# Performance work log

Measured on AMD Instinct MI355X. Metric: run time of the kernel, lower is better.

Reference implementation:

```python
import jax, jax.numpy as jnp
import numpy as np

B, T, V, E, H, NC = 256, 512, 128, 128, 256, 10000


def setup_inputs() -> dict:
    key = jax.random.key(0)
    ks = jax.random.split(key, 10)
    return {
        "dec_input_batch": jax.random.randint(ks[0], (B, T), 0, V),
        "dec_input_lengths": jax.random.randint(ks[1], (B,), 1, T + 1),
        "max_prob_clusters": jax.random.randint(ks[2], (B,), 0, NC),
        "char_embeddings": jax.random.normal(ks[3], (V, E), dtype=jnp.float32) * 0.1,
        "cluster_embeddings": jax.random.normal(ks[4], (NC, H), dtype=jnp.float32) * 0.1,
        "W0": jax.random.normal(ks[5], (E + H + H, 4 * H), dtype=jnp.float32) * 0.05,
        "b0": jnp.zeros((4 * H,), jnp.float32),
        "W1": jax.random.normal(ks[6], (H + H, 4 * H), dtype=jnp.float32) * 0.05,
        "b1": jnp.zeros((4 * H,), jnp.float32),
        "decoderW": jax.random.normal(ks[7], (H, V), dtype=jnp.float32) * (1.0 / (H + V)),
        "decoderB": jnp.zeros((V,), jnp.float32),
    }


def _lstm_step(c, h, x, W, b):
    # TF BasicLSTMCell: gates order i, j, f, o; forget_bias = 1.0
    z = jnp.concatenate([x, h], axis=-1) @ W + b
    i, j, f, o = jnp.split(z, 4, axis=-1)
    c2 = c * jax.nn.sigmoid(f + 1.0) + jax.nn.sigmoid(i) * jnp.tanh(j)
    h2 = jnp.tanh(c2) * jax.nn.sigmoid(o)
    return c2, h2


def reference(dec_input_batch, dec_input_lengths, max_prob_clusters,
              char_embeddings, cluster_embeddings, W0, b0, W1, b1,
              decoderW, decoderB):
    Bb, Tt = dec_input_batch.shape
    Hh = decoderW.shape[0]
    x = char_embeddings[dec_input_batch]                       # [B,T,E]
    clus = cluster_embeddings[max_prob_clusters]               # [B,H]
    clus_bt = jnp.broadcast_to(clus[:, None, :], (Bb, Tt, clus.shape[-1]))
    x = jnp.concatenate([x, clus_bt], axis=-1)                 # [B,T,E+H]
    xs = jnp.transpose(x, (1, 0, 2))                           # [T,B,E+H]
    # dynamic_rnn sequence_length semantics: past length -> zero output, state copied through
    mask = (jnp.arange(Tt)[:, None] < dec_input_lengths[None, :])[..., None]  # [T,B,1]
    zeros = jnp.zeros((Bb, Hh), x.dtype)

    def step(carry, inp):
        c0, h0, c1, h1 = carry
        xt, m = inp
        c0n, h0n = _lstm_step(c0, h0, xt, W0, b0)
        c1n, h1n = _lstm_step(c1, h1, h0n, W1, b1)
        c0 = jnp.where(m, c0n, c0); h0 = jnp.where(m, h0n, h0)
        c1 = jnp.where(m, c1n, c1); h1 = jnp.where(m, h1n, h1)
        out = jnp.where(m, h1n, jnp.zeros_like(h1n))
        return (c0, h0, c1, h1), out

    _, outs = jax.lax.scan(step, (zeros, zeros, zeros, zeros), (xs, mask))
    outs = jnp.transpose(outs, (1, 0, 2))                      # [B,T,H]
    raw_scores = outs @ decoderW + decoderB                    # [B,T,V]
    return raw_scores
```

## Files before the change

### kernel.cpp

```cpp
#include <hip/hip_runtime.h>

#define B_ 256
#define T_ 512
#define V_ 128
#define E_ 128
#define H_ 256
#define FH 1024

#define GROUPS 32
#define RPG 8
#define CWG 16
#define NWG (GROUPS*CWG)

#define HTG 2048
#define GST (GROUPS*HTG)

typedef float f4 __attribute__((ext_vector_type(4)));

#define OFF_HT0  0
#define OFF_HT1  (OFF_HT0 + 2*GST)
#define OFF_BAR  (OFF_HT1 + 2*GST)
#define BARSZ    (GROUPS*1024)
#define OFF_TP   (OFF_BAR + BARSZ)
#define OFF_CP   (OFF_TP + V_*FH)
#define OFF_WP0  (OFF_CP + B_*FH)
#define OFF_WP1  (OFF_WP0 + CWG*64*64*4)
#define OFF_DWT  (OFF_WP1 + CWG*128*64*4)
#define OFF_B1   (OFF_DWT + V_*H_)
#define OFF_PERM (OFF_B1 + FH)

__device__ __forceinline__ int gcol(int c, int col) {
  int u = col >> 2, g = col & 3;
  return g*256 + c*16 + u;
}

__device__ __forceinline__ float sigm(float x){ return 1.f/(1.f+__expf(-x)); }
__device__ __forceinline__ float tanh_(float x){ return 1.f - 2.f/(1.f+__expf(2.f*x)); }


__global__ void prep_pack(const float* __restrict__ W0, const float* __restrict__ W1,
                          const float* __restrict__ dW, const float* __restrict__ b1,
                          float* __restrict__ ws) {
  float* wp0 = ws + OFF_WP0; float* wp1 = ws + OFF_WP1;
  float* dwT = ws + OFF_DWT; float* b1p = ws + OFF_B1;
  const int N0 = CWG*64*64*4;
  const int N1 = CWG*128*64*4;
  const int N2 = V_*H_;
  const int N3 = FH;
  const int total = N0+N1+N2+N3;
  for (int i = blockIdx.x*blockDim.x + threadIdx.x; i < total; i += gridDim.x*blockDim.x) {
    if (i < N0) {
      int cc = i >> 14; int rem = i & 16383;
      int kb = rem >> 8; int ln = (rem >> 2) & 63; int j = i & 3;
      int k = kb*4 + j;
      wp0[i] = W0[(E_+H_+k)*FH + gcol(cc, ln)];
    } else if (i < N0+N1) {
      int idx = i - N0;
      int cc = idx >> 15; int rem = idx & 32767;
      int kb = rem >> 8; int ln = (rem >> 2) & 63; int j = idx & 3;
      int k2 = kb*4 + j;
      wp1[idx] = W1[k2*FH + gcol(cc, ln)];
    } else if (i < N0+N1+N2) {
      int l = i - N0 - N1;
      int v = l >> 8, k = l & 255;
      dwT[l] = dW[k*V_ + v];
    } else {
      int cc2 = i - N0 - N1 - N2;
      b1p[cc2] = b1[gcol(cc2>>6, cc2&63)];
    }
  }
}

__global__ void prep_tok(const float* __restrict__ cemb, const float* __restrict__ W0,
                         float* __restrict__ ws) {
  __shared__ float ce[E_];
  float* TP = ws + OFF_TP;
  int v = blockIdx.x >> 2, q = blockIdx.x & 3;
  int tid = threadIdx.x;
  if (tid < E_) ce[tid] = cemb[v*E_ + tid];
  __syncthreads();
  int ccol = q*256 + tid;
  int G = gcol(ccol>>6, ccol&63);
  float acc = 0.f;
  for (int e = 0; e < E_; ++e) acc = fmaf(ce[e], W0[e*FH + G], acc);
  TP[v*FH + ccol] = acc;
}

__global__ void prep_clus(const int* __restrict__ clus, const float* __restrict__ clemb,
                          const float* __restrict__ W0, const float* __restrict__ b0,
                          float* __restrict__ ws) {
  __shared__ float ce[H_];
  float* CP = ws + OFF_CP;
  int b = blockIdx.x >> 2, q = blockIdx.x & 3;
  int tid = threadIdx.x;
  int cl = clus[b];
  ce[tid] = clemb[(long long)cl*H_ + tid];
  __syncthreads();
  int ccol = q*256 + tid;
  int G = gcol(ccol>>6, ccol&63);
  float acc = b0[G];
  for (int e = 0; e < H_; ++e) acc = fmaf(ce[e], W0[(E_+e)*FH + G], acc);
  CP[b*FH + ccol] = acc;
}

__global__ void prep_sort(const int* __restrict__ lens, float* __restrict__ ws) {
  __shared__ int sl[B_];
  int* perm = (int*)(ws + OFF_PERM);
  const int i = threadIdx.x;
  sl[i] = lens[i];
  __syncthreads();
  const int li = sl[i];
  int rank = 0;
  for (int j = 0; j < B_; ++j) {
    const int lj = sl[j];
    rank += (lj > li) || (lj == li && j < i);
  }
  perm[rank] = i;
}


__device__ __forceinline__ void st64(float* p, float a, float b) {
  float2 t; t.x = a; t.y = b;
  __hip_atomic_store((unsigned long long*)p, __builtin_bit_cast(unsigned long long, t),
                     __ATOMIC_RELAXED, __HIP_MEMORY_SCOPE_AGENT);
}

__device__ __forceinline__ unsigned long long ld64(const void* p) {
  return __hip_atomic_load((const unsigned long long*)p, __ATOMIC_RELAXED,
                           __HIP_MEMORY_SCOPE_AGENT);
}

__device__ __forceinline__ void flag_set(unsigned* p, unsigned v) {
  asm volatile("s_waitcnt vmcnt(0)" ::: "memory");
  __hip_atomic_store(p, v, __ATOMIC_RELAXED, __HIP_MEMORY_SCOPE_AGENT);
}

__device__ __forceinline__ void spinAB(const unsigned* fgrp, int lane, unsigned tgt) {
  const unsigned* p = fgrp + (lane & 15)*32 + ((lane >> 5) << 4);
  unsigned v = __hip_atomic_load(p, __ATOMIC_RELAXED, __HIP_MEMORY_SCOPE_AGENT);
  while (!__all((int)(v >= tgt))) {
    __builtin_amdgcn_s_sleep(4);
    v = __hip_atomic_load(p, __ATOMIC_RELAXED, __HIP_MEMORY_SCOPE_AGENT);
  }
}

__device__ __forceinline__ void spinB(const unsigned* fgrp, int lane, unsigned tgt) {
  const unsigned* p = fgrp + (lane & 15)*32 + 16;
  unsigned v = __hip_atomic_load(p, __ATOMIC_RELAXED, __HIP_MEMORY_SCOPE_AGENT);
  while (!__all((int)(v >= tgt))) {
    __builtin_amdgcn_s_sleep(4);
    v = __hip_atomic_load(p, __ATOMIC_RELAXED, __HIP_MEMORY_SCOPE_AGENT);
  }
}

__device__ __forceinline__ void lstm_gate(const f4 z, float& cc, float& hh, const bool upd) {
  float ci = sigm(z.x);
  float cj = tanh_(z.y);
  float cf = sigm(z.z + 1.f);
  float co = sigm(z.w);
  float cn = fmaf(cc, cf, ci*cj);
  float hn = tanh_(cn)*co;
  if (upd) { cc = cn; hh = hn; }
}


__global__ __launch_bounds__(256, 2) void lstm_persist(
    const int* __restrict__ toks, const int* __restrict__ lens,
    const float* __restrict__ decB, float* __restrict__ ws, float* __restrict__ out)
{
  const int blk  = blockIdx.x;
  const int xcd  = blk & 7;
  const int j    = blk >> 3;
  const int grp  = (xcd << 2) | ((j & 1) << 1) | (j >> 5);
  const int c    = (j >> 1) & 15;
  const int tid  = threadIdx.x;
  const int lane = tid & 63;
  const int wv   = tid >> 6;
  const int cof  = c*64;

  const int sgrp  = ((grp & 3) << 3) | (grp >> 2);
  const int rbase = sgrp*RPG;
  const int* perm = (const int*)(ws + OFF_PERM);

  float* ht0 = ws + OFF_HT0;
  float* ht1 = ws + OFF_HT1;
  unsigned* fgrp = (unsigned*)(ws + OFF_BAR) + grp*1024;
  const float* TP   = ws + OFF_TP;
  const float* CP   = ws + OFF_CP;
  const float* wp0c = ws + OFF_WP0 + c*(64*64*4);
  const float* wp1c = ws + OFF_WP1 + c*(128*64*4);
  const float* dwT  = ws + OFF_DWT;
  const float* b1p  = ws + OFF_B1;

  __shared__ __align__(16) float h0s[2048];
  __shared__ __align__(16) float h1s[2048];
  __shared__ __align__(16) float za[4][8][64];
  __shared__ __align__(16) float zb[4][8][64];
  __shared__ float ldsW[8][260];
  __shared__ float pred[4][64];

  for (int i = tid; i < 8*H_; i += 256)
    ldsW[i>>8][i&255] = dwT[(c*8 + (i>>8))*H_ + (i&255)];

  int Lg = lens[perm[rbase + (lane & 7)]];
  Lg = max(Lg, __shfl_xor(Lg, 1));
  Lg = max(Lg, __shfl_xor(Lg, 2));
  Lg = max(Lg, __shfl_xor(Lg, 4));

  const int gu = lane & 15, q = lane >> 4;
  const int rowA = perm[rbase + q], rowB = perm[rbase + q + 4];
  const int lenA = lens[rowA], lenB = lens[rowB];
  const int* tokApt = toks + rowA*T_;
  const int* tokBpt = toks + rowB*T_;
  const f4 cpA = *(const f4*)(CP + rowA*FH + cof + gu*4);
  const f4 cpB = *(const f4*)(CP + rowB*FH + cof + gu*4);
  const f4 b1v = *(const f4*)(b1p + cof + gu*4);
  const int puboff = grp*HTG + (c*16 + gu)*8 + q*2;
  float c0A = 0.f, h0A = 0.f, c0B = 0.f, h0B = 0.f;
  float c1A = 0.f, h1A = 0.f, c1B = 0.f, h1B = 0.f;

  const int pm = lane >> 3, pv = lane & 7;
  const int prm = (pm < 4) ? pm*2 : (pm-4)*2 + 1;
  const int prow = perm[rbase + pm];
  const int plen = lens[prow];
  const float decb = decB[c*8 + pv];
  float* outp = out + (size_t)prow*T_*V_ + c*8 + pv;

  __syncthreads();

  if (wv == 0) {
    f4 zAv = *(const f4*)(TP + tokApt[0]*FH + cof + gu*4) + cpA;
    f4 zBv = *(const f4*)(TP + tokBpt[0]*FH + cof + gu*4) + cpB;
    lstm_gate(zAv, c0A, h0A, 0 < lenA);
    lstm_gate(zBv, c0B, h0B, 0 < lenB);
    st64(ht0 + puboff, h0A, h0B);
    if (lane == 0) flag_set(fgrp + c*32, 1u);
  } else if (wv == 1) {
    if (lane == 0) flag_set(fgrp + c*32 + 16, 1u);
  }

  for (int t = 0; t < Lg; ++t) {
    const int buf = t & 1;

    f4 tpA = {0,0,0,0}, tpB = {0,0,0,0};
    if (wv == 0 && t + 1 < Lg) {
      tpA = *(const f4*)(TP + tokApt[t+1]*FH + cof + gu*4);
      tpB = *(const f4*)(TP + tokBpt[t+1]*FH + cof + gu*4);
    }

    if (wv == 0) spinAB(fgrp, lane, (unsigned)(t + 1));
    __syncthreads();
    __atomic_signal_fence(__ATOMIC_SEQ_CST);

    {
      const float* s0 = ht0 + buf*GST + grp*HTG + wv*512 + lane*8;
      const float* s1 = ht1 + buf*GST + grp*HTG + wv*512 + lane*8;
      unsigned long long a0 = ld64(s0),   a1 = ld64(s0+2);
      unsigned long long a2 = ld64(s0+4), a3 = ld64(s0+6);
      unsigned long long b0 = ld64(s1),   b1 = ld64(s1+2);
      unsigned long long b2 = ld64(s1+4), b3 = ld64(s1+6);
      float* d0 = h0s + wv*512 + lane*8;
      float* d1 = h1s + wv*512 + lane*8;
      *(unsigned long long*)(d0)   = a0; *(unsigned long long*)(d0+2) = a1;
      *(unsigned long long*)(d0+4) = a2; *(unsigned long long*)(d0+6) = a3;
      *(unsigned long long*)(d1)   = b0; *(unsigned long long*)(d1+2) = b1;
      *(unsigned long long*)(d1+4) = b2; *(unsigned long long*)(d1+6) = b3;
    }

    f4 A0l = {0,0,0,0}, A0h = {0,0,0,0}, A1l = {0,0,0,0}, A1h = {0,0,0,0};
    #pragma unroll 2
    for (int b = 0; b < 16; ++b) {
      const int kb = wv*16 + b;
      const f4 w0 = *(const f4*)(wp0c + kb*256 + lane*4);
      const f4 wl = *(const f4*)(wp1c + kb*256 + lane*4);
      const f4 wu = *(const f4*)(wp1c + (64 + kb)*256 + lane*4);
      #pragma unroll
      for (int jj = 0; jj < 4; ++jj) {
        const int k = kb*4 + jj;
        const float* hb0 = h0s + k*8;
        const float* hb1 = h1s + k*8;
        const f4 h0lo = *(const f4*)(hb0);
        const f4 h0hi = *(const f4*)(hb0 + 4);
        const f4 h1lo = *(const f4*)(hb1);
        const f4 h1hi = *(const f4*)(hb1 + 4);
        const float w0j = w0[jj], wlj = wl[jj], wuj = wu[jj];
        A0l += w0j * h0lo;  A0h += w0j * h0hi;
        A1l += wlj * h0lo + wuj * h1lo;
        A1h += wlj * h0hi + wuj * h1hi;
      }
    }

    float pacc = 0.f;
    {
      const int kq = wv*64;
      #pragma unroll 4
      for (int k2 = 0; k2 < 64; k2 += 4) {
        const f4 w4 = *(const f4*)&ldsW[pv][kq + k2];
        pacc = fmaf(h1s[(kq+k2  )*8 + prm], w4.x, pacc);
        pacc = fmaf(h1s[(kq+k2+1)*8 + prm], w4.y, pacc);
        pacc = fmaf(h1s[(kq+k2+2)*8 + prm], w4.z, pacc);
        pacc = fmaf(h1s[(kq+k2+3)*8 + prm], w4.w, pacc);
      }
    }

    #pragma unroll
    for (int r = 0; r < 4; ++r) {
      za[wv][r][lane]     = A0l[r];
      za[wv][4 + r][lane] = A0h[r];
      zb[wv][r][lane]     = A1l[r];
      zb[wv][4 + r][lane] = A1h[r];
    }
    pred[wv][lane] = pacc;
    __syncthreads();

    if (wv == 0) {
      if (t + 1 < Lg) {
        f4 zA = *(const f4*)&za[0][q*2][gu*4];
        zA += *(const f4*)&za[1][q*2][gu*4];
        zA += *(const f4*)&za[2][q*2][gu*4];
        zA += *(const f4*)&za[3][q*2][gu*4];
        f4 zB = *(const f4*)&za[0][q*2+1][gu*4];
        zB += *(const f4*)&za[1][q*2+1][gu*4];
        zB += *(const f4*)&za[2][q*2+1][gu*4];
        zB += *(const f4*)&za[3][q*2+1][gu*4];
        zA += tpA + cpA;
        zB += tpB + cpB;
        lstm_gate(zA, c0A, h0A, (t+1) < lenA);
        lstm_gate(zB, c0B, h0B, (t+1) < lenB);
        st64(ht0 + (buf^1)*GST + puboff, h0A, h0B);
        if (lane == 0) flag_set(fgrp + c*32, (unsigned)(t + 2));
      }
    } else if (wv == 1) {
      f4 zA = *(const f4*)&zb[0][q*2][gu*4];
      zA += *(const f4*)&zb[1][q*2][gu*4];
      zA += *(const f4*)&zb[2][q*2][gu*4];
      zA += *(const f4*)&zb[3][q*2][gu*4];
      f4 zB = *(const f4*)&zb[0][q*2+1][gu*4];
      zB += *(const f4*)&zb[1][q*2+1][gu*4];
      zB += *(const f4*)&zb[2][q*2+1][gu*4];
      zB += *(const f4*)&zb[3][q*2+1][gu*4];
      zA += b1v;
      zB += b1v;
      lstm_gate(zA, c1A, h1A, t < lenA);
      lstm_gate(zB, c1B, h1B, t < lenB);
      st64(ht1 + (buf^1)*GST + puboff, h1A, h1B);
      if (lane == 0) flag_set(fgrp + c*32 + 16, (unsigned)(t + 2));
    } else if (wv == 2) {
      if (t > 0) {
        float tot = pred[0][lane] + pred[1][lane] + pred[2][lane] + pred[3][lane] + decb;
        if (t - 1 < plen) outp[(size_t)(t-1)*V_] = tot;
      }
    }
  }

  if (wv == 0) spinB(fgrp, lane, (unsigned)(Lg + 1));
  __syncthreads();
  __atomic_signal_fence(__ATOMIC_SEQ_CST);
  {
    const float* s1 = ht1 + (size_t)(Lg & 1)*GST + grp*HTG + wv*512 + lane*8;
    unsigned long long b0 = ld64(s1),   b1 = ld64(s1+2);
    unsigned long long b2 = ld64(s1+4), b3 = ld64(s1+6);
    float* d1 = h1s + wv*512 + lane*8;
    *(unsigned long long*)(d1)   = b0; *(unsigned long long*)(d1+2) = b1;
    *(unsigned long long*)(d1+4) = b2; *(unsigned long long*)(d1+6) = b3;
  }
  {
    float pacc = 0.f;
    const int kq = wv*64;
    #pragma unroll 4
    for (int k2 = 0; k2 < 64; k2 += 4) {
      const f4 w4 = *(const f4*)&ldsW[pv][kq + k2];
      pacc = fmaf(h1s[(kq+k2  )*8 + prm], w4.x, pacc);
      pacc = fmaf(h1s[(kq+k2+1)*8 + prm], w4.y, pacc);
      pacc = fmaf(h1s[(kq+k2+2)*8 + prm], w4.z, pacc);
      pacc = fmaf(h1s[(kq+k2+3)*8 + prm], w4.w, pacc);
    }
    pred[wv][lane] = pacc;
  }
  __syncthreads();
  if (wv == 2) {
    float tot = pred[0][lane] + pred[1][lane] + pred[2][lane] + pred[3][lane] + decb;
    if (Lg - 1 < plen) outp[(size_t)(Lg-1)*V_] = tot;
  }
}


extern "C" void kernel_launch(void* const* d_in, const int* in_sizes, int n_in,
                              void* d_out, int out_size, void* d_ws, size_t ws_size,
                              hipStream_t stream) {
  const int*   toks  = (const int*)d_in[0];
  const int*   lens  = (const int*)d_in[1];
  const int*   clus  = (const int*)d_in[2];
  const float* cemb  = (const float*)d_in[3];
  const float* clemb = (const float*)d_in[4];
  const float* W0    = (const float*)d_in[5];
  const float* b0    = (const float*)d_in[6];
  const float* W1    = (const float*)d_in[7];
  const float* b1    = (const float*)d_in[8];
  const float* dW    = (const float*)d_in[9];
  const float* decB  = (const float*)d_in[10];
  float* out = (float*)d_out;
  float* ws  = (float*)d_ws;

  hipMemsetAsync(out, 0, (size_t)B_*T_*V_*sizeof(float), stream);
  hipMemsetAsync(ws, 0, (size_t)(OFF_BAR + BARSZ)*sizeof(float), stream);

  prep_pack<<<1024, 256, 0, stream>>>(W0, W1, dW, b1, ws);
  prep_tok <<<V_*4, 256, 0, stream>>>(cemb, W0, ws);
  prep_clus<<<B_*4, 256, 0, stream>>>(clus, clemb, W0, b0, ws);
  prep_sort<<<1, 256, 0, stream>>>(lens, ws);
  lstm_persist<<<NWG, 256, 0, stream>>>(toks, lens, decB, ws, out);
}
```

Measured before the change: 4.857 ms.

## Use XCC-local sc0 cache-scope loads/stores for intra-group sync when co-located

At startup each workgroup records its XCC id, and each group checks whether all 16 of its workgroups sit on the same XCC. If they do, the hidden-state exchange and flag signalling use sc0-scoped global loads and stores (shared L2 within one XCC) in place of agent-scope atomics. The spin loop falls back to an agent-scope load every eighth iteration as a safety net. The aim is lower latency on each per-timestep cross-workgroup barrier, but this only helps if the scheduler actually co-locates a group's workgroups, and correctness then depends on L2 coherence within the XCC.

```diff
diff --git a/kernel.cpp b/kernel.cpp
--- a/kernel.cpp
+++ b/kernel.cpp
@@ -16,6 +16,7 @@
 #define GST (GROUPS*HTG)
 
 typedef float f4 __attribute__((ext_vector_type(4)));
+typedef unsigned long long ull;
 
 #define OFF_HT0  0
 #define OFF_HT1  (OFF_HT0 + 2*GST)
@@ -121,18 +122,35 @@
 
 __device__ __forceinline__ void st64(float* p, float a, float b) {
   float2 t; t.x = a; t.y = b;
-  __hip_atomic_store((unsigned long long*)p, __builtin_bit_cast(unsigned long long, t),
+  __hip_atomic_store((ull*)p, __builtin_bit_cast(ull, t),
                      __ATOMIC_RELAXED, __HIP_MEMORY_SCOPE_AGENT);
 }
 
-__device__ __forceinline__ unsigned long long ld64(const void* p) {
-  return __hip_atomic_load((const unsigned long long*)p, __ATOMIC_RELAXED,
-                           __HIP_MEMORY_SCOPE_AGENT);
+__device__ __forceinline__ void st64_sc0(float* p, float a, float b) {
+  float2 t; t.x = a; t.y = b;
+  ull v = __builtin_bit_cast(ull, t);
+  asm volatile("global_store_dwordx2 %0, %1, off sc0" :: "v"(p), "v"(v) : "memory");
+}
+
+__device__ __forceinline__ ull ld64(const void* p) {
+  return __hip_atomic_load((const ull*)p, __ATOMIC_RELAXED, __HIP_MEMORY_SCOPE_AGENT);
+}
+
+__device__ __forceinline__ unsigned ld32_sc0(const unsigned* p) {
+  unsigned v;
+  asm volatile("global_load_dword %0, %1, off sc0\n\t"
+               "s_waitcnt vmcnt(0)"
+               : "=v"(v) : "v"(p) : "memory");
+  return v;
 }
 
 __device__ __forceinline__ void flag_set(unsigned* p, unsigned v) {
   asm volatile("s_waitcnt vmcnt(0)" ::: "memory");
   __hip_atomic_store(p, v, __ATOMIC_RELAXED, __HIP_MEMORY_SCOPE_AGENT);
+}
+__device__ __forceinline__ void flag_set_sc0(unsigned* p, unsigned v) {
+  asm volatile("s_waitcnt vmcnt(0)" ::: "memory");
+  asm volatile("global_store_dword %0, %1, off sc0" :: "v"(p), "v"(v) : "memory");
 }
 
 __device__ __forceinline__ void spinAB(const unsigned* fgrp, int lane, unsigned tgt) {
@@ -141,6 +159,17 @@
   while (!__all((int)(v >= tgt))) {
     __builtin_amdgcn_s_sleep(4);
     v = __hip_atomic_load(p, __ATOMIC_RELAXED, __HIP_MEMORY_SCOPE_AGENT);
+  }
+}
+__device__ __forceinline__ void spinAB_fast(const unsigned* fgrp, int lane, unsigned tgt) {
+  const unsigned* p = fgrp + (lane & 15)*32 + ((lane >> 5) << 4);
+  unsigned v = ld32_sc0(p);
+  int it = 0;
+  while (!__all((int)(v >= tgt))) {
+    __builtin_amdgcn_s_sleep(4);
+    ++it;
+    v = (it & 7) ? ld32_sc0(p)
+                 : __hip_atomic_load(p, __ATOMIC_RELAXED, __HIP_MEMORY_SCOPE_AGENT);
   }
 }
 
@@ -198,9 +227,25 @@
   __shared__ __align__(16) float zb[4][8][64];
   __shared__ float ldsW[8][260];
   __shared__ float pred[4][64];
+  __shared__ unsigned fastSh;
 
   for (int i = tid; i < 8*H_; i += 256)
     ldsW[i>>8][i&255] = dwT[(c*8 + (i>>8))*H_ + (i&255)];
+
+  unsigned xcc;
+  asm volatile("s_getreg_b32 %0, hwreg(HW_REG_XCC_ID)" : "=s"(xcc));
+  if (tid == 0)
+    __hip_atomic_store(fgrp + 512 + c, xcc + 1u, __ATOMIC_RELAXED, __HIP_MEMORY_SCOPE_AGENT);
+  if (wv == 0) {
+    const unsigned* p = fgrp + 512 + (lane & 15);
+    unsigned v = __hip_atomic_load(p, __ATOMIC_RELAXED, __HIP_MEMORY_SCOPE_AGENT);
+    while (!__all((int)(v != 0u))) {
+      __builtin_amdgcn_s_sleep(8);
+      v = __hip_atomic_load(p, __ATOMIC_RELAXED, __HIP_MEMORY_SCOPE_AGENT);
+    }
+    const bool same = __all((int)(v == xcc + 1u));
+    if (lane == 0) fastSh = same ? 1u : 0u;
+  }
 
   int Lg = lens[perm[rbase + (lane & 7)]];
   Lg = max(Lg, __shfl_xor(Lg, 1));
@@ -227,16 +272,24 @@
   float* outp = out + (size_t)prow*T_*V_ + c*8 + pv;
 
   __syncthreads();
+  const bool fast = (fastSh != 0u);
 
   if (wv == 0) {
     f4 zAv = *(const f4*)(TP + tokApt[0]*FH + cof + gu*4) + cpA;
     f4 zBv = *(const f4*)(TP + tokBpt[0]*FH + cof + gu*4) + cpB;
     lstm_gate(zAv, c0A, h0A, 0 < lenA);
     lstm_gate(zBv, c0B, h0B, 0 < lenB);
-    st64(ht0 + puboff, h0A, h0B);
-    if (lane == 0) flag_set(fgrp + c*32, 1u);
+    if (fast) st64_sc0(ht0 + puboff, h0A, h0B);
+    else      st64(ht0 + puboff, h0A, h0B);
+    if (lane == 0) {
+      if (fast) flag_set_sc0(fgrp + c*32, 1u);
+      else      flag_set(fgrp + c*32, 1u);
+    }
   } else if (wv == 1) {
-    if (lane == 0) flag_set(fgrp + c*32 + 16, 1u);
+    if (lane == 0) {
+      if (fast) flag_set_sc0(fgrp + c*32 + 16, 1u);
+      else      flag_set(fgrp + c*32 + 16, 1u);
+    }
   }
 
   for (int t = 0; t < Lg; ++t) {
@@ -248,23 +301,40 @@
       tpB = *(const f4*)(TP + tokBpt[t+1]*FH + cof + gu*4);
     }
 
-    if (wv == 0) spinAB(fgrp, lane, (unsigned)(t + 1));
+    if (wv == 0) {
+      if (fast) spinAB_fast(fgrp, lane, (unsigned)(t + 1));
+      else      spinAB(fgrp, lane, (unsigned)(t + 1));
+    }
     __syncthreads();
     __atomic_signal_fence(__ATOMIC_SEQ_CST);
 
     {
       const float* s0 = ht0 + buf*GST + grp*HTG + wv*512 + lane*8;
       const float* s1 = ht1 + buf*GST + grp*HTG + wv*512 + lane*8;
-      unsigned long long a0 = ld64(s0),   a1 = ld64(s0+2);
-      unsigned long long a2 = ld64(s0+4), a3 = ld64(s0+6);
-      unsigned long long b0 = ld64(s1),   b1 = ld64(s1+2);
-      unsigned long long b2 = ld64(s1+4), b3 = ld64(s1+6);
+      ull a0, a1, a2, a3, c0, c1, c2, c3;
+      if (fast) {
+        asm volatile(
+          "global_load_dwordx2 %0, %8, off sc0\n\t"
+          "global_load_dwordx2 %1, %8, off offset:8 sc0\n\t"
+          "global_load_dwordx2 %2, %8, off offset:16 sc0\n\t"
+          "global_load_dwordx2 %3, %8, off offset:24 sc0\n\t"
+          "global_load_dwordx2 %4, %9, off sc0\n\t"
+          "global_load_dwordx2 %5, %9, off offset:8 sc0\n\t"
+          "global_load_dwordx2 %6, %9, off offset:16 sc0\n\t"
+          "global_load_dwordx2 %7, %9, off offset:24 sc0\n\t"
+          "s_waitcnt vmcnt(0)"
+          : "=&v"(a0), "=&v"(a1), "=&v"(a2), "=&v"(a3),
+            "=&v"(c0), "=&v"(c1), "=&v"(c2), "=&v"(c3)
+          : "v"(s0), "v"(s1)
+          : "memory");
+      } else {
+        a0 = ld64(s0);   a1 = ld64(s0+2); a2 = ld64(s0+4); a3 = ld64(s0+6);
+        c0 = ld64(s1);   c1 = ld64(s1+2); c2 = ld64(s1+4); c3 = ld64(s1+6);
+      }
       float* d0 = h0s + wv*512 + lane*8;
       float* d1 = h1s + wv*512 + lane*8;
-      *(unsigned long long*)(d0)   = a0; *(unsigned long long*)(d0+2) = a1;
-      *(unsigned long long*)(d0+4) = a2; *(unsigned long long*)(d0+6) = a3;
-      *(unsigned long long*)(d1)   = b0; *(unsigned long long*)(d1+2) = b1;
-      *(unsigned long long*)(d1+4) = b2; *(unsigned long long*)(d1+6) = b3;
+      *(ull*)(d0)   = a0; *(ull*)(d0+2) = a1; *(ull*)(d0+4) = a2; *(ull*)(d0+6) = a3;
+      *(ull*)(d1)   = c0; *(ull*)(d1+2) = c1; *(ull*)(d1+4) = c2; *(ull*)(d1+6) = c3;
     }
 
     f4 A0l = {0,0,0,0}, A0h = {0,0,0,0}, A1l = {0,0,0,0}, A1h = {0,0,0,0};
@@ -327,8 +397,13 @@
         zB += tpB + cpB;
         lstm_gate(zA, c0A, h0A, (t+1) < lenA);
         lstm_gate(zB, c0B, h0B, (t+1) < lenB);
-        st64(ht0 + (buf^1)*GST + puboff, h0A, h0B);
-        if (lane == 0) flag_set(fgrp + c*32, (unsigned)(t + 2));
+        float* pb = ht0 + (buf^1)*GST + puboff;
+        if (fast) st64_sc0(pb, h0A, h0B);
+        else      st64(pb, h0A, h0B);
+        if (lane == 0) {
+          if (fast) flag_set_sc0(fgrp + c*32, (unsigned)(t + 2));
+          else      flag_set(fgrp + c*32, (unsigned)(t + 2));
+        }
       }
     } else if (wv == 1) {
       f4 zA = *(const f4*)&zb[0][q*2][gu*4];
@@ -343,8 +418,13 @@
       zB += b1v;
       lstm_gate(zA, c1A, h1A, t < lenA);
       lstm_gate(zB, c1B, h1B, t < lenB);
-      st64(ht1 + (buf^1)*GST + puboff, h1A, h1B);
-      if (lane == 0) flag_set(fgrp + c*32 + 16, (unsigned)(t + 2));
+      float* pb = ht1 + (buf^1)*GST + puboff;
+      if (fast) st64_sc0(pb, h1A, h1B);
+      else      st64(pb, h1A, h1B);
+      if (lane == 0) {
+        if (fast) flag_set_sc0(fgrp + c*32 + 16, (unsigned)(t + 2));
+        else      flag_set(fgrp + c*32 + 16, (unsigned)(t + 2));
+      }
     } else if (wv == 2) {
       if (t > 0) {
         float tot = pred[0][lane] + pred[1][lane] + pred[2][lane] + pred[3][lane] + decb;
@@ -358,11 +438,11 @@
   __atomic_signal_fence(__ATOMIC_SEQ_CST);
   {
     const float* s1 = ht1 + (size_t)(Lg & 1)*GST + grp*HTG + wv*512 + lane*8;
-    unsigned long long b0 = ld64(s1),   b1 = ld64(s1+2);
-    unsigned long long b2 = ld64(s1+4), b3 = ld64(s1+6);
+    ull b0 = ld64(s1),   b1 = ld64(s1+2);
+    ull b2 = ld64(s1+4), b3 = ld64(s1+6);
     float* d1 = h1s + wv*512 + lane*8;
-    *(unsigned long long*)(d1)   = b0; *(unsigned long long*)(d1+2) = b1;
-    *(unsigned long long*)(d1+4) = b2; *(unsigned long long*)(d1+6) = b3;
+    *(ull*)(d1)   = b0; *(ull*)(d1+2) = b1;
+    *(ull*)(d1+4) = b2; *(ull*)(d1+6) = b3;
   }
   {
     float pacc = 0.f;
```

New measurement: 4.931 ms. About the same (+1.5%).
